# Kernel tuning notes

Measured on AMD Instinct MI355X. Metric: run time of the kernel, lower is better.

Reference implementation:

```python
import jax, jax.numpy as jnp
import numpy as np

B, T, H = 64, 512, 1024


def setup_inputs() -> dict:
    key = jax.random.key(0)
    k1, k2, k3 = jax.random.split(key, 3)
    # xavier-normal for W_ih (std = sqrt(2/(fan_in+fan_out)))
    std_ih = np.sqrt(2.0 / (3 * H + H)).astype(np.float32)
    W_ih = jax.random.normal(k1, (3 * H, H), dtype=jnp.float32) * std_ih
    # orthogonal-ish init for W_hh (scaled normal is fine for a numeric baseline)
    W_hh = jax.random.normal(k2, (3 * H, H), dtype=jnp.float32) / np.sqrt(H).astype(np.float32)
    return {
        "m_enc": jax.random.normal(k3, (B, T, H), dtype=jnp.float32),
        "W_ih": W_ih,
        "W_hh": W_hh,
        "b_ih": jnp.zeros((3 * H,), jnp.float32),
        "b_hh": jnp.zeros((3 * H,), jnp.float32),
    }


def reference(m_enc, W_ih, W_hh, b_ih, b_hh):
    # m_enc: [B, T, H]; GRUCell with hidden size H, h0 = zeros.
    b, t, h = m_enc.shape
    # Precompute input projections for all timesteps in one big GEMM: [B, T, 3H]
    gi = jnp.einsum('bth,gh->btg', m_enc, W_ih) + b_ih

    def step(h_prev, gi_t):
        gh = h_prev @ W_hh.T + b_hh  # [B, 3H]
        i_r, i_z, i_n = jnp.split(gi_t, 3, axis=-1)
        h_r, h_z, h_n = jnp.split(gh, 3, axis=-1)
        r = jax.nn.sigmoid(i_r + h_r)
        z = jax.nn.sigmoid(i_z + h_z)
        n = jnp.tanh(i_n + r * h_n)
        h_new = (1.0 - z) * n + z * h_prev
        return h_new, h_new

    h0 = jnp.zeros((b, h), m_enc.dtype)
    _, ys = jax.lax.scan(step, h0, jnp.swapaxes(gi, 0, 1))  # ys: [T, B, H]
    return jnp.swapaxes(ys, 0, 1)  # [B, T, H]
```

## Files before the change

### kernel.cpp

```cpp
#include <hip/hip_runtime.h>
#include <hip/hip_bf16.h>

#define B_ 64
#define T_ 512
#define H_ 1024
#define G_ 3072
#define M_ (B_ * T_)

typedef __attribute__((ext_vector_type(8))) short bf16x8;
typedef __attribute__((ext_vector_type(4))) float f32x4;

__device__ __forceinline__ unsigned short f2bf(float x) {
  __hip_bfloat16 h = __float2bfloat16(x);
  return *reinterpret_cast<unsigned short*>(&h);
}
__device__ __forceinline__ float bf2f(unsigned short u) {
  __hip_bfloat16 h;
  *reinterpret_cast<unsigned short*>(&h) = u;
  return __bfloat162float(h);
}

__global__ __launch_bounds__(256) void cvt_f32_to_bf16(const float* __restrict__ src,
                                                       unsigned short* __restrict__ dst,
                                                       long n) {
  long i = ((long)blockIdx.x * 256 + threadIdx.x) * 4;
  if (i + 4 <= n) {
    float4 v = *(const float4*)(src + i);
    ushort4 o;
    o.x = f2bf(v.x); o.y = f2bf(v.y); o.z = f2bf(v.z); o.w = f2bf(v.w);
    *(ushort4*)(dst + i) = o;
  }
}

__global__ __launch_bounds__(256) void gemm_nt_bf16(const unsigned short* __restrict__ A,
                                                    const unsigned short* __restrict__ Bw,
                                                    const float* __restrict__ bias,
                                                    unsigned short* __restrict__ C) {
  constexpr int BM = 128, BN = 128, BK = 64;
  constexpr int K = H_, N = G_;
  __shared__ unsigned short As[BM * BK];
  __shared__ unsigned short Bs[BN * BK];
  const int nbn = N / BN;
  const int bn = blockIdx.x % nbn;
  const int bm = blockIdx.x / nbn;
  const int tid = threadIdx.x;
  const int wave = tid >> 6;
  const int lane = tid & 63;
  const int l15 = lane & 15, l4 = lane >> 4;
  const int wr = wave >> 1, wc = wave & 1;

  const long a0 = (long)bm * BM;
  const long b0 = (long)bn * BN;

  f32x4 acc[4][4] = {};

  const int srow = tid >> 3;
  const int schk = tid & 7;

  for (int k0 = 0; k0 < K; k0 += BK) {
#pragma unroll
    for (int r = 0; r < 4; ++r) {
      int row = r * 32 + srow;
      const unsigned short* ga = A + (a0 + row) * K + k0 + schk * 8;
      const unsigned short* gb = Bw + (b0 + row) * K + k0 + schk * 8;
      char* la = (char*)As + r * 4096 + wave * 1024;
      char* lb = (char*)Bs + r * 4096 + wave * 1024;
      __builtin_amdgcn_global_load_lds((const __attribute__((address_space(1))) void*)ga,
                                       (__attribute__((address_space(3))) void*)la, 16, 0, 0);
      __builtin_amdgcn_global_load_lds((const __attribute__((address_space(1))) void*)gb,
                                       (__attribute__((address_space(3))) void*)lb, 16, 0, 0);
    }
    __syncthreads();
#pragma unroll
    for (int kk = 0; kk < BK; kk += 32) {
      bf16x8 af[4], bfr[4];
#pragma unroll
      for (int i = 0; i < 4; ++i)
        af[i] = *(const bf16x8*)&As[(wr * 64 + i * 16 + l15) * BK + kk + l4 * 8];
#pragma unroll
      for (int j = 0; j < 4; ++j)
        bfr[j] = *(const bf16x8*)&Bs[(wc * 64 + j * 16 + l15) * BK + kk + l4 * 8];
#pragma unroll
      for (int i = 0; i < 4; ++i)
#pragma unroll
        for (int j = 0; j < 4; ++j)
          acc[i][j] = __builtin_amdgcn_mfma_f32_16x16x32_bf16(af[i], bfr[j], acc[i][j], 0, 0, 0);
    }
    __syncthreads();
  }
#pragma unroll
  for (int j = 0; j < 4; ++j) {
    int col = (int)b0 + wc * 64 + j * 16 + l15;
    float bv = bias[col];
#pragma unroll
    for (int i = 0; i < 4; ++i) {
      long row = a0 + wr * 64 + i * 16 + l4 * 4;
#pragma unroll
      for (int r2 = 0; r2 < 4; ++r2) {
        C[(row + r2) * N + col] = f2bf(acc[i][j][r2] + bv);
      }
    }
  }
}

__global__ __launch_bounds__(256) void gru_step(const unsigned short* __restrict__ hprev_bf,
                                                unsigned short* __restrict__ hout_bf,
                                                const unsigned short* __restrict__ Whh,
                                                const unsigned short* __restrict__ gi,
                                                const float* __restrict__ b_hh,
                                                float* __restrict__ out,
                                                int t) {
  const int blk = blockIdx.x;
  const int c0 = blk * 4;
  const int tid = threadIdx.x;
  const int wave = tid >> 6;
  const int lane = tid & 63;
  const int l15 = lane & 15, l4 = lane >> 4;

  const int gsel = l15 >> 2;
  const int gcol = c0 + (l15 & 3);
  const long brow = (gsel < 3) ? ((long)gsel * H_ + gcol) : (long)gcol;
  const unsigned short* bptr = Whh + brow * H_ + l4 * 8;
  const unsigned short* aptr = hprev_bf + (long)(wave * 16 + l15) * H_ + l4 * 8;

  f32x4 acc0 = {}, acc1 = {}, acc2 = {}, acc3 = {};
#pragma unroll 4
  for (int kk = 0; kk < H_; kk += 128) {
    bf16x8 a0v = *(const bf16x8*)(aptr + kk);
    bf16x8 b0v = *(const bf16x8*)(bptr + kk);
    bf16x8 a1v = *(const bf16x8*)(aptr + kk + 32);
    bf16x8 b1v = *(const bf16x8*)(bptr + kk + 32);
    bf16x8 a2v = *(const bf16x8*)(aptr + kk + 64);
    bf16x8 b2v = *(const bf16x8*)(bptr + kk + 64);
    bf16x8 a3v = *(const bf16x8*)(aptr + kk + 96);
    bf16x8 b3v = *(const bf16x8*)(bptr + kk + 96);
    acc0 = __builtin_amdgcn_mfma_f32_16x16x32_bf16(a0v, b0v, acc0, 0, 0, 0);
    acc1 = __builtin_amdgcn_mfma_f32_16x16x32_bf16(a1v, b1v, acc1, 0, 0, 0);
    acc2 = __builtin_amdgcn_mfma_f32_16x16x32_bf16(a2v, b2v, acc2, 0, 0, 0);
    acc3 = __builtin_amdgcn_mfma_f32_16x16x32_bf16(a3v, b3v, acc3, 0, 0, 0);
  }
  f32x4 acc = (acc0 + acc1) + (acc2 + acc3);

  __shared__ float gh[64][12];
  if (l15 < 12) {
#pragma unroll
    for (int r = 0; r < 4; ++r)
      gh[wave * 16 + l4 * 4 + r][l15] = acc[r];
  }
  __syncthreads();

  const int b = tid >> 2;
  const int cc = tid & 3;
  const int col = c0 + cc;
  float ghr = gh[b][cc] + b_hh[col];
  float ghz = gh[b][4 + cc] + b_hh[H_ + col];
  float ghn = gh[b][8 + cc] + b_hh[2 * H_ + col];
  const long gib = ((long)b * T_ + t) * G_;
  float gir = bf2f(gi[gib + col]);
  float giz = bf2f(gi[gib + H_ + col]);
  float gin = bf2f(gi[gib + 2 * H_ + col]);
  float hp = (t == 0) ? 0.f : out[((long)b * T_ + (t - 1)) * H_ + col];
  float rg = 1.f / (1.f + __expf(-(gir + ghr)));
  float zg = 1.f / (1.f + __expf(-(giz + ghz)));
  float pre = gin + rg * ghn;
  float ng = 2.f / (1.f + __expf(-2.f * pre)) - 1.f;
  float hn = (1.f - zg) * ng + zg * hp;
  out[((long)b * T_ + t) * H_ + col] = hn;
  hout_bf[(long)b * H_ + col] = f2bf(hn);
}

extern "C" void kernel_launch(void* const* d_in, const int* in_sizes, int n_in,
                              void* d_out, int out_size, void* d_ws, size_t ws_size,
                              hipStream_t stream) {
  const float* m_enc = (const float*)d_in[0];
  const float* W_ih = (const float*)d_in[1];
  const float* W_hh = (const float*)d_in[2];
  const float* b_ih = (const float*)d_in[3];
  const float* b_hh = (const float*)d_in[4];
  float* out = (float*)d_out;

  const size_t off_A = 0;
  const size_t off_Wih = off_A + (size_t)M_ * H_ * 2;
  const size_t off_Whh = off_Wih + (size_t)G_ * H_ * 2;
  const size_t off_gi = off_Whh + (size_t)G_ * H_ * 2;
  const size_t off_h0 = off_gi + (size_t)M_ * G_ * 2;
  const size_t off_h1 = off_h0 + (size_t)B_ * H_ * 2;
  const size_t need = off_h1 + (size_t)B_ * H_ * 2;
  if (ws_size < need) return;

  char* ws = (char*)d_ws;
  unsigned short* A_bf = (unsigned short*)(ws + off_A);
  unsigned short* Wih_bf = (unsigned short*)(ws + off_Wih);
  unsigned short* Whh_bf = (unsigned short*)(ws + off_Whh);
  unsigned short* gi_bf = (unsigned short*)(ws + off_gi);
  unsigned short* h0 = (unsigned short*)(ws + off_h0);
  unsigned short* h1 = (unsigned short*)(ws + off_h1);

  cvt_f32_to_bf16<<<(int)((size_t)M_ * H_ / 1024), 256, 0, stream>>>(m_enc, A_bf, (long)M_ * H_);
  cvt_f32_to_bf16<<<(int)((size_t)G_ * H_ / 1024), 256, 0, stream>>>(W_ih, Wih_bf, (long)G_ * H_);
  cvt_f32_to_bf16<<<(int)((size_t)G_ * H_ / 1024), 256, 0, stream>>>(W_hh, Whh_bf, (long)G_ * H_);

  gemm_nt_bf16<<<(M_ / 128) * (G_ / 128), 256, 0, stream>>>(A_bf, Wih_bf, b_ih, gi_bf);

  hipMemsetAsync(h0, 0, (size_t)B_ * H_ * 2, stream);
  for (int t = 0; t < T_; ++t) {
    unsigned short* hr = (t & 1) ? h1 : h0;
    unsigned short* hw = (t & 1) ? h0 : h1;
    gru_step<<<H_ / 4, 256, 0, stream>>>(hr, hw, Whh_bf, gi_bf, b_hh, out, t);
  }
}
```

Baseline: 6.524 ms.

## Widen GRU step blocks to 16 columns with three gate accumulators in registers

The per-timestep GRU kernel now gives each block 16 hidden columns instead of 4, launching 64 blocks instead of 256. Each wave keeps separate r/z/n MFMA accumulators, so one load of the hidden-state fragment feeds three MFMAs. Lanes now map directly to (batch, column) outputs, which removes the shared-memory transpose and the block barrier. The gi loads are issued before the matmul loop to hide their latency. The cost is far fewer blocks per step (64 on a large GPU), so memory parallelism for streaming W_hh each step may drop.

```diff
diff --git a/kernel.cpp b/kernel.cpp
--- a/kernel.cpp
+++ b/kernel.cpp
@@ -103,70 +103,63 @@
   }
 }
 
-__global__ __launch_bounds__(256) void gru_step(const unsigned short* __restrict__ hprev_bf,
-                                                unsigned short* __restrict__ hout_bf,
-                                                const unsigned short* __restrict__ Whh,
-                                                const unsigned short* __restrict__ gi,
-                                                const float* __restrict__ b_hh,
-                                                float* __restrict__ out,
-                                                int t) {
-  const int blk = blockIdx.x;
-  const int c0 = blk * 4;
+__global__ __launch_bounds__(256) void gru_step64(const unsigned short* __restrict__ hprev_bf,
+                                                  unsigned short* __restrict__ hout_bf,
+                                                  const unsigned short* __restrict__ Whh,
+                                                  const unsigned short* __restrict__ gi,
+                                                  const float* __restrict__ b_hh,
+                                                  float* __restrict__ out,
+                                                  int t) {
+  const int c0 = blockIdx.x * 16;
   const int tid = threadIdx.x;
   const int wave = tid >> 6;
   const int lane = tid & 63;
   const int l15 = lane & 15, l4 = lane >> 4;
 
-  const int gsel = l15 >> 2;
-  const int gcol = c0 + (l15 & 3);
-  const long brow = (gsel < 3) ? ((long)gsel * H_ + gcol) : (long)gcol;
-  const unsigned short* bptr = Whh + brow * H_ + l4 * 8;
-  const unsigned short* aptr = hprev_bf + (long)(wave * 16 + l15) * H_ + l4 * 8;
-
-  f32x4 acc0 = {}, acc1 = {}, acc2 = {}, acc3 = {};
-#pragma unroll 4
-  for (int kk = 0; kk < H_; kk += 128) {
-    bf16x8 a0v = *(const bf16x8*)(aptr + kk);
-    bf16x8 b0v = *(const bf16x8*)(bptr + kk);
-    bf16x8 a1v = *(const bf16x8*)(aptr + kk + 32);
-    bf16x8 b1v = *(const bf16x8*)(bptr + kk + 32);
-    bf16x8 a2v = *(const bf16x8*)(aptr + kk + 64);
-    bf16x8 b2v = *(const bf16x8*)(bptr + kk + 64);
-    bf16x8 a3v = *(const bf16x8*)(aptr + kk + 96);
-    bf16x8 b3v = *(const bf16x8*)(bptr + kk + 96);
-    acc0 = __builtin_amdgcn_mfma_f32_16x16x32_bf16(a0v, b0v, acc0, 0, 0, 0);
-    acc1 = __builtin_amdgcn_mfma_f32_16x16x32_bf16(a1v, b1v, acc1, 0, 0, 0);
-    acc2 = __builtin_amdgcn_mfma_f32_16x16x32_bf16(a2v, b2v, acc2, 0, 0, 0);
-    acc3 = __builtin_amdgcn_mfma_f32_16x16x32_bf16(a3v, b3v, acc3, 0, 0, 0);
-  }
-  f32x4 acc = (acc0 + acc1) + (acc2 + acc3);
-
-  __shared__ float gh[64][12];
-  if (l15 < 12) {
-#pragma unroll
-    for (int r = 0; r < 4; ++r)
-      gh[wave * 16 + l4 * 4 + r][l15] = acc[r];
-  }
-  __syncthreads();
-
-  const int b = tid >> 2;
-  const int cc = tid & 3;
-  const int col = c0 + cc;
-  float ghr = gh[b][cc] + b_hh[col];
-  float ghz = gh[b][4 + cc] + b_hh[H_ + col];
-  float ghn = gh[b][8 + cc] + b_hh[2 * H_ + col];
-  const long gib = ((long)b * T_ + t) * G_;
-  float gir = bf2f(gi[gib + col]);
-  float giz = bf2f(gi[gib + H_ + col]);
-  float gin = bf2f(gi[gib + 2 * H_ + col]);
-  float hp = (t == 0) ? 0.f : out[((long)b * T_ + (t - 1)) * H_ + col];
-  float rg = 1.f / (1.f + __expf(-(gir + ghr)));
-  float zg = 1.f / (1.f + __expf(-(giz + ghz)));
-  float pre = gin + rg * ghn;
-  float ng = 2.f / (1.f + __expf(-2.f * pre)) - 1.f;
-  float hn = (1.f - zg) * ng + zg * hp;
-  out[((long)b * T_ + t) * H_ + col] = hn;
-  hout_bf[(long)b * H_ + col] = f2bf(hn);
+  const int col = c0 + l15;
+  const int bb0 = wave * 16 + l4 * 4;
+
+  const unsigned short* ap = hprev_bf + (size_t)(wave * 16 + l15) * H_ + l4 * 8;
+  const unsigned short* bpr = Whh + (size_t)(0 * H_ + c0 + l15) * H_ + l4 * 8;
+  const unsigned short* bpz = Whh + (size_t)(1 * H_ + c0 + l15) * H_ + l4 * 8;
+  const unsigned short* bpn = Whh + (size_t)(2 * H_ + c0 + l15) * H_ + l4 * 8;
+
+  unsigned short gr[4], gz[4], gn[4];
+#pragma unroll
+  for (int r = 0; r < 4; ++r) {
+    long gib = ((long)(bb0 + r) * T_ + t) * G_;
+    gr[r] = gi[gib + col];
+    gz[r] = gi[gib + H_ + col];
+    gn[r] = gi[gib + 2 * H_ + col];
+  }
+  const float bhr = b_hh[col];
+  const float bhz = b_hh[H_ + col];
+  const float bhn = b_hh[2 * H_ + col];
+
+  f32x4 accr = {}, accz = {}, accn = {};
+#pragma unroll 8
+  for (int kk = 0; kk < H_; kk += 32) {
+    bf16x8 a = *(const bf16x8*)(ap + kk);
+    bf16x8 br = *(const bf16x8*)(bpr + kk);
+    bf16x8 bz = *(const bf16x8*)(bpz + kk);
+    bf16x8 bn2 = *(const bf16x8*)(bpn + kk);
+    accr = __builtin_amdgcn_mfma_f32_16x16x32_bf16(a, br, accr, 0, 0, 0);
+    accz = __builtin_amdgcn_mfma_f32_16x16x32_bf16(a, bz, accz, 0, 0, 0);
+    accn = __builtin_amdgcn_mfma_f32_16x16x32_bf16(a, bn2, accn, 0, 0, 0);
+  }
+
+#pragma unroll
+  for (int r = 0; r < 4; ++r) {
+    int b = bb0 + r;
+    float hp = (t == 0) ? 0.f : out[((long)b * T_ + (t - 1)) * H_ + col];
+    float rg = 1.f / (1.f + __expf(-(bf2f(gr[r]) + accr[r] + bhr)));
+    float zg = 1.f / (1.f + __expf(-(bf2f(gz[r]) + accz[r] + bhz)));
+    float pre = bf2f(gn[r]) + rg * (accn[r] + bhn);
+    float ng = 2.f / (1.f + __expf(-2.f * pre)) - 1.f;
+    float hn = (1.f - zg) * ng + zg * hp;
+    out[((long)b * T_ + t) * H_ + col] = hn;
+    hout_bf[(size_t)b * H_ + col] = f2bf(hn);
+  }
 }
 
 extern "C" void kernel_launch(void* const* d_in, const int* in_sizes, int n_in,
@@ -206,6 +199,6 @@
   for (int t = 0; t < T_; ++t) {
     unsigned short* hr = (t & 1) ? h1 : h0;
     unsigned short* hw = (t & 1) ? h0 : h1;
-    gru_step<<<H_ / 4, 256, 0, stream>>>(hr, hw, Whh_bf, gi_bf, b_hh, out, t);
-  }
-}
+    gru_step64<<<64, 256, 0, stream>>>(hr, hw, Whh_bf, gi_bf, b_hh, out, t);
+  }
+}
```

After: 9.803 ms. 50.3% more time.
